# Performance work log

Hardware: AMD Instinct MI355X
Metric: run time of the kernel (lower is better)

The kernel has to match this reference:

```python
import jax, jax.numpy as jnp
import numpy as np

K = 64          # neighbours (output has K+1 columns incl. self)
RADIUS = -1.0   # <=0 means no radius cutoff (module default)


def setup_inputs() -> dict:
    key = jax.random.key(0)
    B, S, D = 8, 4096, 4  # 8 events of 4096 points, 4 coord dims
    coordinates = jax.random.normal(key, (B * S, D), dtype=jnp.float32)
    row_splits = (jnp.arange(B + 1) * S).astype(jnp.int32)  # equal ragged splits
    return {"coordinates": coordinates, "row_splits": row_splits}


def _knn(coordinates, row_splits):
    B = row_splits.shape[0] - 1
    N, D = coordinates.shape
    S = N // B  # equal-size segments (static under jit)
    c = coordinates.reshape(B, S, D)
    # squared pairwise distances per segment: [B, S, S]
    sq = jnp.sum(c * c, axis=-1)
    d2 = sq[:, :, None] + sq[:, None, :] - 2.0 * jnp.einsum('bsd,btd->bst', c, c)
    d2 = jnp.maximum(d2, 0.0)
    # K+1 smallest squared distances (self has d2=0, comes first)
    neg_vals, idx = jax.lax.top_k(-d2, K + 1)      # [B, S, K+1]
    dist = -neg_vals
    # local -> global indices via segment offsets
    idx = idx + (jnp.arange(B, dtype=idx.dtype) * S)[:, None, None]
    idx = idx.reshape(N, K + 1)
    dist = dist.reshape(N, K + 1)
    if RADIUS > 0:
        # SelectKnn squares max_radius; out-of-radius -> idx=-1, dist=0
        m = dist <= RADIUS * RADIUS
        idx = jnp.where(m, idx, -1)
        dist = jnp.where(m, dist, 0.0)
    return idx, dist


def reference(coordinates, row_splits):
    return _knn(coordinates, row_splits)
```

## Files before the change

### kernel.cpp

```cpp
#include <hip/hip_runtime.h>
#include <hip/hip_bf16.h>
#include <stdint.h>

#pragma clang fp contract(off)

#define KOUT 65
#define CAP  128
#define QPB  8
#define HALF 2048


__device__ __forceinline__ void wave_lds_sync() {
  asm volatile("s_waitcnt lgkmcnt(0)" ::: "memory");
  __builtin_amdgcn_wave_barrier();
}

__device__ __forceinline__ float sq_ref(const float4 c) {
  float p0 = c.x * c.x, p1 = c.y * c.y, p2 = c.z * c.z, p3 = c.w * c.w;
  return (p0 + p2) + (p1 + p3);
}

__device__ __forceinline__ float d2_ref(const float4 q, const float4 c,
                                        const float qs) {
  const float cs = sq_ref(c);
  const float dot = __builtin_fmaf(c.w, q.w,
                    __builtin_fmaf(c.z, q.z,
                    __builtin_fmaf(c.y, q.y,
                    __builtin_fmaf(c.x, q.x, 0.0f))));
  const float s = qs + cs;
  const float d2 = __builtin_fmaf(-2.0f, dot, s);
  return fmaxf(d2, 0.0f);
}

__global__ __launch_bounds__(512) void knn_kernel(
    const float* __restrict__ coords, float* __restrict__ out,
    int N, int S) {
  __shared__ float4 sc[HALF];
  __shared__ unsigned long long buf[QPB][CAP];

  const int tid  = threadIdx.x;
  const int lane = tid & 63;
  const int w    = tid >> 6;
  const int qi   = blockIdx.x * QPB + w;
  const int base = ((blockIdx.x * QPB) / S) * S;

  const float4* c4 = (const float4*)coords;
  const float4 q = c4[qi < N ? qi : 0];
  const float qs = sq_ref(q);

  float d2v[64];
#pragma unroll
  for (int h = 0; h < 2; ++h) {
    __syncthreads();
#pragma unroll
    for (int it = 0; it < HALF / 512; ++it) {
      const int k = it * 512 + tid;
      sc[k] = c4[base + h * HALF + k];
    }
    __syncthreads();
#pragma unroll
    for (int tt = 0; tt < 32; ++tt) {
      d2v[h * 32 + tt] = d2_ref(q, sc[tt * 64 + lane], qs);
    }
  }

  if (qi >= N) return;

  float lo = 0.0f;
  float hi = -1.0f;
  float tau = 0.2612f * __expf(0.25f * qs);
  float tau_sel = -1.0f;
  int   my_cnt = 0;
  bool  have = false;
  for (int it = 0; it < 24; ++it) {
    int cl = 0;
#pragma unroll
    for (int t = 0; t < 64; ++t) cl += (d2v[t] <= tau) ? 1 : 0;
    int c = cl;
#pragma unroll
    for (int off = 32; off; off >>= 1) c += __shfl_xor(c, off, 64);

    if (c >= KOUT) {
      if (tau_sel < 0.0f || tau < tau_sel) tau_sel = tau;
      if (c <= CAP) { my_cnt = cl; have = true; break; }
      hi = tau;
    } else {
      lo = tau;
    }
    float prop = tau * __builtin_sqrtf(90.0f / (float)(c > 0 ? c : 1));
    bool bad = !(prop > lo) || (hi >= 0.0f && !(prop < hi));
    if (bad) prop = (hi >= 0.0f) ? 0.5f * (lo + hi) : tau * 2.0f;
    tau = prop;
  }
  float taueff;
  if (have) {
    taueff = tau_sel;
  } else {
    taueff = (tau_sel >= 0.0f) ? tau_sel : 3.0e38f;
    my_cnt = 0;
#pragma unroll
    for (int t = 0; t < 64; ++t) my_cnt += (d2v[t] <= taueff) ? 1 : 0;
  }

  int pre = my_cnt;
#pragma unroll
  for (int off = 1; off < 64; off <<= 1) {
    const int y = __shfl_up(pre, off, 64);
    if (lane >= off) pre += y;
  }
  const int myoff = pre - my_cnt;

#pragma unroll
  for (int b = 0; b < CAP / 64; ++b) buf[w][b * 64 + lane] = ~0ULL;
  wave_lds_sync();

  int o = myoff;
#pragma unroll
  for (int t = 0; t < 64; ++t) {
    if (d2v[t] <= taueff) {
      if (o < CAP) {
        const unsigned int bits = __float_as_uint(d2v[t]);
        buf[w][o] =
            ((unsigned long long)bits << 32) | (unsigned int)(t * 64 + lane);
      }
      ++o;
    }
  }
  wave_lds_sync();

  unsigned long long val[2];
#pragma unroll
  for (int e = 0; e < 2; ++e) val[e] = buf[w][e * 64 + lane];
  wave_lds_sync();

#pragma unroll
  for (int k = 2; k <= CAP; k <<= 1) {
    for (int j = k >> 1; j; j >>= 1) {
      if (j >= 64) {
        const unsigned i0 = (unsigned)lane;
        const bool asc = ((i0 & (unsigned)k) == 0u);
        const unsigned long long a = val[0], b2 = val[1];
        if ((a > b2) == asc) { val[0] = b2; val[1] = a; }
      } else {
#pragma unroll
        for (int e = 0; e < 2; ++e) {
          const unsigned long long other = __shfl_xor(val[e], j, 64);
          const unsigned i = (unsigned)e * 64u + (unsigned)lane;
          const bool asc = ((i & (unsigned)k) == 0u);
          const bool upper = (lane & j) != 0;
          const bool keep_max = (asc == upper);
          const bool gt = val[e] > other;
          val[e] = (gt == keep_max) ? val[e] : other;
        }
      }
    }
  }

  const long long NK = (long long)N * KOUT;
  {
    const unsigned long long v = val[0];
    out[(long long)qi * KOUT + lane] = (float)(base + (int)(v & 0xffffffffu));
    out[NK + (long long)qi * KOUT + lane] =
        __uint_as_float((unsigned int)(v >> 32));
    if (lane == 0) {
      const unsigned long long v64 = val[1];
      out[(long long)qi * KOUT + 64] = (float)(base + (int)(v64 & 0xffffffffu));
      out[NK + (long long)qi * KOUT + 64] =
          __uint_as_float((unsigned int)(v64 >> 32));
    }
  }
}

extern "C" void kernel_launch(void* const* d_in, const int* in_sizes, int n_in,
                              void* d_out, int out_size, void* d_ws, size_t ws_size,
                              hipStream_t stream) {
  const float* coords = (const float*)d_in[0];
  const int N = in_sizes[0] / 4;
  const int B = in_sizes[1] - 1;
  const int S = N / B;
  const int blocks = (N + QPB - 1) / QPB;
  knn_kernel<<<blocks, 512, 0, stream>>>(coords, (float*)d_out, N, S);
}
```

Before: 227.8 us.

## Launch one wave per query and read candidates directly from global memory

Replaces the 8-query blocks that staged each segment half into shared memory with single-wave blocks, one per query. Each lane loads its candidate points from global memory in groups of eight and computes distances directly. This removes the block-wide barriers and the large shared-memory tile, which should raise occupancy. In exchange, every query re-reads the full segment through the cache hierarchy instead of sharing one staged copy.

```diff
diff --git a/kernel.cpp b/kernel.cpp
--- a/kernel.cpp
+++ b/kernel.cpp
@@ -6,8 +6,7 @@
 
 #define KOUT 65
 #define CAP  128
-#define QPB  8
-#define HALF 2048
+#define GRP  8
 
 
 __device__ __forceinline__ void wave_lds_sync() {
@@ -32,39 +31,31 @@
   return fmaxf(d2, 0.0f);
 }
 
-__global__ __launch_bounds__(512) void knn_kernel(
+__global__ __launch_bounds__(64) void knn_kernel(
     const float* __restrict__ coords, float* __restrict__ out,
     int N, int S) {
-  __shared__ float4 sc[HALF];
-  __shared__ unsigned long long buf[QPB][CAP];
+  __shared__ unsigned long long buf[CAP];
 
-  const int tid  = threadIdx.x;
-  const int lane = tid & 63;
-  const int w    = tid >> 6;
-  const int qi   = blockIdx.x * QPB + w;
-  const int base = ((blockIdx.x * QPB) / S) * S;
+  const int lane = threadIdx.x;
+  const int qi   = blockIdx.x;
+  if (qi >= N) return;
+  const int base = (qi / S) * S;
 
   const float4* c4 = (const float4*)coords;
-  const float4 q = c4[qi < N ? qi : 0];
+  const float4 q = c4[qi];
   const float qs = sq_ref(q);
 
   float d2v[64];
+#pragma unroll 1
+  for (int g = 0; g < 64 / GRP; ++g) {
+    float4 cc[GRP];
 #pragma unroll
-  for (int h = 0; h < 2; ++h) {
-    __syncthreads();
+    for (int j = 0; j < GRP; ++j)
+      cc[j] = c4[base + (g * GRP + j) * 64 + lane];
 #pragma unroll
-    for (int it = 0; it < HALF / 512; ++it) {
-      const int k = it * 512 + tid;
-      sc[k] = c4[base + h * HALF + k];
-    }
-    __syncthreads();
-#pragma unroll
-    for (int tt = 0; tt < 32; ++tt) {
-      d2v[h * 32 + tt] = d2_ref(q, sc[tt * 64 + lane], qs);
-    }
+    for (int j = 0; j < GRP; ++j)
+      d2v[g * GRP + j] = d2_ref(q, cc[j], qs);
   }
-
-  if (qi >= N) return;
 
   float lo = 0.0f;
   float hi = -1.0f;
@@ -111,7 +102,7 @@
   const int myoff = pre - my_cnt;
 
 #pragma unroll
-  for (int b = 0; b < CAP / 64; ++b) buf[w][b * 64 + lane] = ~0ULL;
+  for (int b = 0; b < CAP / 64; ++b) buf[b * 64 + lane] = ~0ULL;
   wave_lds_sync();
 
   int o = myoff;
@@ -120,7 +111,7 @@
     if (d2v[t] <= taueff) {
       if (o < CAP) {
         const unsigned int bits = __float_as_uint(d2v[t]);
-        buf[w][o] =
+        buf[o] =
             ((unsigned long long)bits << 32) | (unsigned int)(t * 64 + lane);
       }
       ++o;
@@ -130,7 +121,7 @@
 
   unsigned long long val[2];
 #pragma unroll
-  for (int e = 0; e < 2; ++e) val[e] = buf[w][e * 64 + lane];
+  for (int e = 0; e < 2; ++e) val[e] = buf[e * 64 + lane];
   wave_lds_sync();
 
 #pragma unroll
@@ -178,6 +169,5 @@
   const int N = in_sizes[0] / 4;
   const int B = in_sizes[1] - 1;
   const int S = N / B;
-  const int blocks = (N + QPB - 1) / QPB;
-  knn_kernel<<<blocks, 512, 0, stream>>>(coords, (float*)d_out, N, S);
+  knn_kernel<<<N, 64, 0, stream>>>(coords, (float*)d_out, N, S);
 }
```

Result: slower. 376.2 us (+65.2%).
